# Kernel tuning notes

Hardware: AMD Instinct MI355X
Metric: run time of the kernel (lower is better)

The kernel has to match this reference:

```python
import jax, jax.numpy as jnp
import numpy as np
import math

B, D_MODEL, EMB, ORDER, SEQ = 4, 64, 33, 64, 256
TARGET, FAST_PCT, SLOW_PCT = 0.01, 0.3, 1.5


def _pos_emb(L, emb_dim):
    # PositionalEmbedding: t in [0,1], complex exponential bands
    t = jnp.linspace(0.0, 1.0, L)[None, :, None]                     # [1,L,1]
    bands = (emb_dim - 1) // 2
    t_r = jnp.linspace(0.0, L - 1.0, L)[None, :, None]
    w = 2.0 * math.pi * t_r / L
    f = jnp.linspace(1e-4, bands - 1.0, bands)[None, None]
    zc = jnp.exp(-1j * f * w)
    z = jnp.concatenate([t, zc.real, zc.imag], axis=-1)              # [1,L,emb_dim]
    return z.astype(jnp.float32), t.astype(jnp.float32)


def setup_inputs() -> dict:
    key = jax.random.key(0)
    ks = jax.random.split(key, 24)
    z, _ = _pos_emb(SEQ, EMB)

    def lin(k, fan_in, fan_out):
        return jax.random.normal(k, (fan_in, fan_out), jnp.float32) / np.sqrt(fan_in)

    inp = {
        'x': jax.random.normal(ks[0], (B, D_MODEL, SEQ, SEQ), jnp.float32),
        'z': z,
        'Xw1': lin(ks[1], EMB, ORDER), 'Xb1': jax.random.normal(ks[2], (ORDER,), jnp.float32) * 0.02,
        'Xw2': lin(ks[3], ORDER, ORDER), 'Xb2': jax.random.normal(ks[4], (ORDER,), jnp.float32) * 0.02,
        'Xw3': lin(ks[5], ORDER, ORDER), 'Xb3': jax.random.normal(ks[6], (ORDER,), jnp.float32) * 0.02,
        'Xwo': lin(ks[7], ORDER, D_MODEL),
        'Xfreq': jnp.ones((1, ORDER), jnp.float32),  # Sin freq, w=1, shared across layers
        'Yw1': lin(ks[8], EMB, ORDER), 'Yb1': jax.random.normal(ks[9], (ORDER,), jnp.float32) * 0.02,
        'Yw2': lin(ks[10], ORDER, ORDER), 'Yb2': jax.random.normal(ks[11], (ORDER,), jnp.float32) * 0.02,
        'Yw3': lin(ks[12], ORDER, ORDER), 'Yb3': jax.random.normal(ks[13], (ORDER,), jnp.float32) * 0.02,
        'Ywo': lin(ks[14], ORDER, D_MODEL),
        'Yfreq': jnp.ones((1, ORDER), jnp.float32),
        'bias': jax.random.normal(ks[15], (D_MODEL,), jnp.float32),
        'L': SEQ,
    }
    return inp


def _implicit_filter(z, w1, b1, w2, b2, w3, b3, wo, freq, t, deltas):
    # MLP with shared Sin activation, then exponential modulation (shift=0)
    h = jnp.sin(freq * (z @ w1 + b1))
    h = jnp.sin(freq * (h @ w2 + b2))
    h = jnp.sin(freq * (h @ w3 + b3))
    h = h @ wo                                   # [1,L,d_model]
    decay = jnp.exp(-t * jnp.abs(deltas))        # [1,L,d_model]
    return h * decay


def reference(x, z, Xw1, Xb1, Xw2, Xb2, Xw3, Xb3, Xwo, Xfreq,
              Yw1, Yb1, Yw2, Yb2, Yw3, Yb3, Ywo, Yfreq, bias, L):
    d_model = x.shape[1]
    t = jnp.linspace(0.0, 1.0, L)[None, :, None].astype(jnp.float32)
    max_dec = math.log(TARGET) / FAST_PCT
    min_dec = math.log(TARGET) / SLOW_PCT
    deltas = jnp.linspace(min_dec, max_dec, d_model)[None, None].astype(jnp.float32)

    hx = _implicit_filter(z, Xw1, Xb1, Xw2, Xb2, Xw3, Xb3, Xwo, Xfreq, t, deltas)
    hy = _implicit_filter(z, Yw1, Yb1, Yw2, Yb2, Yw3, Yb3, Ywo, Yfreq, t, deltas)
    # separable outer-product 2D kernel: [1,L,L,d_model] -> [d_model,L,L]
    k = jnp.einsum('ijk,imk->ijmk', hx, hy)[0]
    k = jnp.transpose(k, (2, 0, 1))

    fft_size = 2 * L
    k_f = jnp.fft.rfft2(k, s=(fft_size, fft_size)) / fft_size       # [D, 2L, L+1]
    u_f = jnp.fft.rfft2(x.astype(jnp.float32), s=(fft_size, fft_size))  # [B, D, 2L, L+1]
    y = jnp.fft.irfft2(u_f * k_f, s=(fft_size, fft_size))[..., :L, :L]
    out = y + x * bias[:, None, None]
    return out.astype(x.dtype)
```

## Files before the change

kernel.cpp:

```cpp
#include <hip/hip_runtime.h>

#define SL 256
#define RSTRIDE 312

typedef _Float16 f16;
typedef _Float16 f16x8 __attribute__((ext_vector_type(8)));
typedef _Float16 f16x4 __attribute__((ext_vector_type(4)));
typedef float f32x4 __attribute__((ext_vector_type(4)));

__global__ __launch_bounds__(64) void k_filters(
    const float* __restrict__ z,
    const float* __restrict__ Xw1, const float* __restrict__ Xb1,
    const float* __restrict__ Xw2, const float* __restrict__ Xb2,
    const float* __restrict__ Xw3, const float* __restrict__ Xb3,
    const float* __restrict__ Xwo, const float* __restrict__ Xfreq,
    const float* __restrict__ Yw1, const float* __restrict__ Yb1,
    const float* __restrict__ Yw2, const float* __restrict__ Yb2,
    const float* __restrict__ Yw3, const float* __restrict__ Yb3,
    const float* __restrict__ Ywo, const float* __restrict__ Yfreq,
    f16* __restrict__ hxT, f16* __restrict__ hyT)
{
    const int l = blockIdx.x;
    const int sel = blockIdx.y;
    const int t = threadIdx.x;
    const float* w1 = sel ? Yw1 : Xw1;  const float* b1 = sel ? Yb1 : Xb1;
    const float* w2 = sel ? Yw2 : Xw2;  const float* b2 = sel ? Yb2 : Xb2;
    const float* w3 = sel ? Yw3 : Xw3;  const float* b3 = sel ? Yb3 : Xb3;
    const float* wo = sel ? Ywo : Xwo;  const float* freq = sel ? Yfreq : Xfreq;
    f16* hT = sel ? hyT : hxT;

    __shared__ float zb[33];
    __shared__ float ha[64];
    __shared__ float hb[64];

    if (t < 33) zb[t] = z[l * 33 + t];
    __syncthreads();

    const float fr = freq[t];
    float s = b1[t];
    for (int k = 0; k < 33; ++k) s += zb[k] * w1[k * 64 + t];
    ha[t] = sinf(fr * s);
    __syncthreads();

    s = b2[t];
    for (int k = 0; k < 64; ++k) s += ha[k] * w2[k * 64 + t];
    hb[t] = sinf(fr * s);
    __syncthreads();

    s = b3[t];
    for (int k = 0; k < 64; ++k) s += hb[k] * w3[k * 64 + t];
    ha[t] = sinf(fr * s);
    __syncthreads();

    s = 0.f;
    for (int k = 0; k < 64; ++k) s += ha[k] * wo[k * 64 + t];

    const float MIN_DEC = -3.0701134573253937f;
    const float MAX_DEC = -15.350567286626968f;
    float ad = fabsf(MIN_DEC + (MAX_DEC - MIN_DEC) * ((float)t / 63.0f));
    float tl = (float)l / 255.0f;
    hT[t * 256 + l] = (f16)(s * expf(-tl * ad));
}

__device__ __forceinline__ f16x8 cvt8(float4 a, float4 b)
{
    f16x8 h;
    h[0] = (f16)a.x; h[1] = (f16)a.y; h[2] = (f16)a.z; h[3] = (f16)a.w;
    h[4] = (f16)b.x; h[5] = (f16)b.y; h[6] = (f16)b.z; h[7] = (f16)b.w;
    return h;
}

template<int NT>
__device__ __forceinline__ void build_R(f16* R, const f16* __restrict__ hc,
                                        int tid)
{
    for (int idx = tid; idx < 8 * RSTRIDE; idx += NT) {
        int c = idx / RSTRIDE;
        int k = idx - c * RSTRIDE;
        int u = k + c;
        R[idx] = (u <= 255) ? hc[255 - u] : (f16)0.f;
    }
}

__global__ __launch_bounds__(1024, 4) void k_one(
    const float* __restrict__ x, const f16* __restrict__ hxT,
    const f16* __restrict__ hyT, const float* __restrict__ bias,
    float* __restrict__ out)
{
    extern __shared__ __align__(16) f16 smem[];
    f16* tmp = smem;
    f16* Ry  = smem + 256 * 256;
    f16* Rx  = Ry + 8 * RSTRIDE;

    const int bd = blockIdx.x;
    const int d  = bd & 63;
    const int tid  = threadIdx.x;
    const int lane = tid & 63;
    const int wave = tid >> 6;
    const int ln   = lane & 15;
    const int quad = lane >> 4;

    const float* xbd = x + (size_t)bd * (SL * SL);

    build_R<1024>(Ry, hyT + d * 256, tid);

    f32x4 acc[16];
#pragma unroll
    for (int a = 0; a < 16; ++a) acc[a] = (f32x4){0.f, 0.f, 0.f, 0.f};

    __syncthreads();

    {
        const float* xr = xbd + (wave * 16 + ln) * SL + quad * 8;
        float4 a0 = *(const float4*)xr;
        float4 a1 = *(const float4*)(xr + 4);

#pragma unroll
        for (int s = 0; s < 8; ++s) {
            const int q0 = s * 32;
            f16x8 af = cvt8(a0, a1);
            if (s + 1 < 8) {
                a0 = *(const float4*)(xr + q0 + 32);
                a1 = *(const float4*)(xr + q0 + 36);
            }
#pragma unroll
            for (int c8 = 0; c8 < 16; ++c8) {
                if (32 * s <= c8 * 16 + 15) {
                    int j = c8 * 16 + ln;
                    int s0 = 255 - j + q0 + quad * 8;
                    int c = s0 & 7;
                    f16x8 bf = *(const f16x8*)&Ry[c * RSTRIDE + (s0 - c)];
                    acc[c8] = __builtin_amdgcn_mfma_f32_16x16x32_f16(
                        af, bf, acc[c8], 0, 0, 0);
                }
            }
        }

#pragma unroll
        for (int c8 = 0; c8 < 16; ++c8) {
            int jl = c8 * 16 + ln;
            int pb = wave * 16 + quad * 4;
            f32x4 a = acc[c8];
            f16x4 v;
            v[0] = (f16)a[0]; v[1] = (f16)a[1];
            v[2] = (f16)a[2]; v[3] = (f16)a[3];
            *(f16x4*)&tmp[jl * 256 + (pb ^ ((jl & 7) << 3))] = v;
        }
    }

    build_R<1024>(Rx, hxT + d * 256, tid);
#pragma unroll
    for (int a = 0; a < 16; ++a) acc[a] = (f32x4){0.f, 0.f, 0.f, 0.f};

    __syncthreads();

    const int igrp = wave & 3;
    const int jgrp = wave >> 2;
    const int nst = (igrp + 1) * 2;
    for (int s = 0; s < nst; ++s) {
        const int p0 = s * 32;
        f16x8 af[4];
#pragma unroll
        for (int rt = 0; rt < 4; ++rt) {
            int jl = jgrp * 64 + rt * 16 + ln;
            int off = (p0 + quad * 8) ^ ((jl & 7) << 3);
            af[rt] = *(const f16x8*)&tmp[jl * 256 + off];
        }
#pragma unroll
        for (int ct = 0; ct < 4; ++ct) {
            if (p0 <= igrp * 64 + ct * 16 + 15) {
                int i = igrp * 64 + ct * 16 + ln;
                int s0 = 255 - i + p0 + quad * 8;
                int c = s0 & 7;
                f16x8 bf = *(const f16x8*)&Rx[c * RSTRIDE + (s0 - c)];
#pragma unroll
                for (int rt = 0; rt < 4; ++rt)
                    acc[rt * 4 + ct] = __builtin_amdgcn_mfma_f32_16x16x32_f16(
                        af[rt], bf, acc[rt * 4 + ct], 0, 0, 0);
            }
        }
    }

    const float bv = bias[d];
    const float sc = 1.0f / 512.0f;
    float* obd = out + (size_t)bd * (SL * SL);
#pragma unroll
    for (int rt = 0; rt < 4; ++rt)
#pragma unroll
        for (int ct = 0; ct < 4; ++ct) {
            int i = igrp * 64 + ct * 16 + ln;
            int j = jgrp * 64 + rt * 16 + quad * 4;
            f32x4 a = acc[rt * 4 + ct];
            float4 xv = *(const float4*)(xbd + i * SL + j);
            float4 o;
            o.x = a[0] * sc + xv.x * bv;
            o.y = a[1] * sc + xv.y * bv;
            o.z = a[2] * sc + xv.z * bv;
            o.w = a[3] * sc + xv.w * bv;
            *(float4*)(obd + i * SL + j) = o;
        }
}

template<int J0>
__device__ __forceinline__ void phase1(
    const float* __restrict__ xr0, const float* __restrict__ xr1,
    const f16* __restrict__ R, f32x4 (&acc)[16], int ln, int quad)
{
    constexpr int QS = (J0 == 0) ? 4 : 8;
    float4 a0 = *(const float4*)xr0;
    float4 a1 = *(const float4*)(xr0 + 4);
    float4 b0 = *(const float4*)xr1;
    float4 b1 = *(const float4*)(xr1 + 4);

#pragma unroll
    for (int s = 0; s < QS; ++s) {
        const int q0 = s * 32;
        f16x8 af0 = cvt8(a0, a1);
        f16x8 af1 = cvt8(b0, b1);
        if (s + 1 < QS) {
            a0 = *(const float4*)(xr0 + q0 + 32);
            a1 = *(const float4*)(xr0 + q0 + 36);
            b0 = *(const float4*)(xr1 + q0 + 32);
            b1 = *(const float4*)(xr1 + q0 + 36);
        }
#pragma unroll
        for (int c8 = 0; c8 < 8; ++c8) {
            if (32 * s <= J0 + c8 * 16 + 15) {
                int j = J0 + c8 * 16 + ln;
                int s0 = 255 - j + q0 + quad * 8;
                int c = s0 & 7;
                f16x8 bf = *(const f16x8*)&R[c * RSTRIDE + (s0 - c)];
                acc[c8] = __builtin_amdgcn_mfma_f32_16x16x32_f16(
                    af0, bf, acc[c8], 0, 0, 0);
                acc[8 + c8] = __builtin_amdgcn_mfma_f32_16x16x32_f16(
                    af1, bf, acc[8 + c8], 0, 0, 0);
            }
        }
    }
}

__global__ __launch_bounds__(512, 4) void k_fused(
    const float* __restrict__ x, const f16* __restrict__ hxT,
    const f16* __restrict__ hyT, const float* __restrict__ bias,
    float* __restrict__ out)
{
    const int bd = blockIdx.x & 255;
    const int j0 = (blockIdx.x >> 8) << 7;
    const int d  = bd & 63;
    const int tid  = threadIdx.x;
    const int lane = tid & 63;
    const int wave = tid >> 6;
    const int ln   = lane & 15;
    const int quad = lane >> 4;

    __shared__ __align__(16) f16 tmp[128 * 256];
    __shared__ __align__(16) f16 R[8 * RSTRIDE];

    const float* xbd = x + (size_t)bd * (SL * SL);

    build_R<512>(R, hyT + d * 256, tid);

    f32x4 acc[16];
#pragma unroll
    for (int a = 0; a < 16; ++a) acc[a] = (f32x4){0.f, 0.f, 0.f, 0.f};

    __syncthreads();

    {
        const float* xr0 = xbd + (wave * 32 + ln) * SL + quad * 8;
        const float* xr1 = xr0 + 16 * SL;
        if (j0 == 0) phase1<0>(xr0, xr1, R, acc, ln, quad);
        else         phase1<128>(xr0, xr1, R, acc, ln, quad);

#pragma unroll
        for (int r = 0; r < 2; ++r)
#pragma unroll
            for (int c8 = 0; c8 < 8; ++c8) {
                int jl = c8 * 16 + ln;
                int pb = wave * 32 + r * 16 + quad * 4;
                f32x4 a = acc[r * 8 + c8];
                f16x4 v;
                v[0] = (f16)a[0]; v[1] = (f16)a[1];
                v[2] = (f16)a[2]; v[3] = (f16)a[3];
                *(f16x4*)&tmp[jl * 256 + (pb ^ ((jl & 7) << 3))] = v;
            }
    }

    __syncthreads();
    build_R<512>(R, hxT + d * 256, tid);
#pragma unroll
    for (int a = 0; a < 16; ++a) acc[a] = (f32x4){0.f, 0.f, 0.f, 0.f};
    __syncthreads();

    const int igrp = wave & 3;
    const int jgrp = wave >> 2;
    const int nst = (igrp + 1) * 2;
    for (int s = 0; s < nst; ++s) {
        const int p0 = s * 32;
        f16x8 af[4];
#pragma unroll
        for (int rt = 0; rt < 4; ++rt) {
            int jl = jgrp * 64 + rt * 16 + ln;
            int off = (p0 + quad * 8) ^ ((jl & 7) << 3);
            af[rt] = *(const f16x8*)&tmp[jl * 256 + off];
        }
#pragma unroll
        for (int ct = 0; ct < 4; ++ct) {
            if (p0 <= igrp * 64 + ct * 16 + 15) {
                int i = igrp * 64 + ct * 16 + ln;
                int s0 = 255 - i + p0 + quad * 8;
                int c = s0 & 7;
                f16x8 bf = *(const f16x8*)&R[c * RSTRIDE + (s0 - c)];
#pragma unroll
                for (int rt = 0; rt < 4; ++rt)
                    acc[rt * 4 + ct] = __builtin_amdgcn_mfma_f32_16x16x32_f16(
                        af[rt], bf, acc[rt * 4 + ct], 0, 0, 0);
            }
        }
    }

    const float bv = bias[d];
    const float sc = 1.0f / 512.0f;
    float* obd = out + (size_t)bd * (SL * SL);
#pragma unroll
    for (int rt = 0; rt < 4; ++rt)
#pragma unroll
        for (int ct = 0; ct < 4; ++ct) {
            int i = igrp * 64 + ct * 16 + ln;
            int j = j0 + jgrp * 64 + rt * 16 + quad * 4;
            f32x4 a = acc[rt * 4 + ct];
            float4 xv = *(const float4*)(xbd + i * SL + j);
            float4 o;
            o.x = a[0] * sc + xv.x * bv;
            o.y = a[1] * sc + xv.y * bv;
            o.z = a[2] * sc + xv.z * bv;
            o.w = a[3] * sc + xv.w * bv;
            *(float4*)(obd + i * SL + j) = o;
        }
}

extern "C" void kernel_launch(void* const* d_in, const int* in_sizes, int n_in,
                              void* d_out, int out_size, void* d_ws, size_t ws_size,
                              hipStream_t stream)
{
    (void)in_sizes; (void)n_in; (void)out_size; (void)ws_size;
    const float* x     = (const float*)d_in[0];
    const float* z     = (const float*)d_in[1];
    const float* Xw1   = (const float*)d_in[2];
    const float* Xb1   = (const float*)d_in[3];
    const float* Xw2   = (const float*)d_in[4];
    const float* Xb2   = (const float*)d_in[5];
    const float* Xw3   = (const float*)d_in[6];
    const float* Xb3   = (const float*)d_in[7];
    const float* Xwo   = (const float*)d_in[8];
    const float* Xfreq = (const float*)d_in[9];
    const float* Yw1   = (const float*)d_in[10];
    const float* Yb1   = (const float*)d_in[11];
    const float* Yw2   = (const float*)d_in[12];
    const float* Yb2   = (const float*)d_in[13];
    const float* Yw3   = (const float*)d_in[14];
    const float* Yb3   = (const float*)d_in[15];
    const float* Ywo   = (const float*)d_in[16];
    const float* Yfreq = (const float*)d_in[17];
    const float* bias  = (const float*)d_in[18];

    f16* hxT = (f16*)d_ws;
    f16* hyT = hxT + 64 * 256;

    k_filters<<<dim3(256, 2), 64, 0, stream>>>(
        z, Xw1, Xb1, Xw2, Xb2, Xw3, Xb3, Xwo, Xfreq,
        Yw1, Yb1, Yw2, Yb2, Yw3, Yb3, Ywo, Yfreq, hxT, hyT);

    const int dyn_lds = (256 * 256 + 2 * 8 * RSTRIDE) * (int)sizeof(f16);
    static hipError_t attr_rc = hipFuncSetAttribute(
        (const void*)k_one, hipFuncAttributeMaxDynamicSharedMemorySize, dyn_lds);

    if (attr_rc == hipSuccess) {
        k_one<<<256, 1024, dyn_lds, stream>>>(x, hxT, hyT, bias, (float*)d_out);
    } else {
        k_fused<<<512, 512, 0, stream>>>(x, hxT, hyT, bias, (float*)d_out);
    }
}
```

Measured before the change: 166.8 us.

## Split k_one into two column-chunk phases with double-buffered intermediate

Replaces the single-pass kernel, which ran the full row convolution into a 256x256 LDS buffer and then the full column convolution, with a kernel that processes the output in two 128-column chunks. Each chunk gets its own LDS buffer. Both Toeplitz tables are built up front and the x loads for the next chunk are issued before the current phase-2 work, aiming to overlap global loads with MFMA work. Waves are regrouped into 8 row groups by 2 column groups, which balances the triangular work differently. The cost is more barriers, some x rows loaded twice, and higher register pressure from prefetched data.

```diff
diff --git a/kernel.cpp b/kernel.cpp
--- a/kernel.cpp
+++ b/kernel.cpp
@@ -82,15 +82,104 @@
     }
 }
 
-__global__ __launch_bounds__(1024, 4) void k_one(
+template<int JC>
+__device__ __forceinline__ void p1_work(
+    const f16x8* axs, const f16* __restrict__ Ry, f16* __restrict__ buf,
+    int wave, int ln, int quad)
+{
+    f32x4 acc[8];
+#pragma unroll
+    for (int t = 0; t < 8; ++t) acc[t] = (f32x4){0.f, 0.f, 0.f, 0.f};
+
+#pragma unroll
+    for (int s = 0; s <= 4 * JC + 3; ++s) {
+        const int q0 = s * 32;
+#pragma unroll
+        for (int c8 = 0; c8 < 8; ++c8) {
+            if (s <= 4 * JC + (c8 >> 1)) {
+                const int j = JC * 128 + c8 * 16 + ln;
+                const int s0 = 255 - j + q0 + quad * 8;
+                const int c = s0 & 7;
+                f16x8 bf = *(const f16x8*)&Ry[c * RSTRIDE + (s0 - c)];
+                acc[c8] = __builtin_amdgcn_mfma_f32_16x16x32_f16(
+                    axs[s], bf, acc[c8], 0, 0, 0);
+            }
+        }
+    }
+#pragma unroll
+    for (int c8 = 0; c8 < 8; ++c8) {
+        const int jl = c8 * 16 + ln;
+        const int pb = wave * 16 + quad * 4;
+        f32x4 a = acc[c8];
+        f16x4 v;
+        v[0] = (f16)a[0]; v[1] = (f16)a[1];
+        v[2] = (f16)a[2]; v[3] = (f16)a[3];
+        *(f16x4*)&buf[jl * 256 + (pb ^ ((jl & 7) << 3))] = v;
+    }
+}
+
+template<int JC>
+__device__ __forceinline__ void p2_chunk(
+    const f16* __restrict__ buf, const f16* __restrict__ Rx,
+    const float* __restrict__ xbd, float* __restrict__ obd, float bv,
+    int igrp, int jgrp, int ln, int quad)
+{
+    f32x4 acc[8];
+#pragma unroll
+    for (int t = 0; t < 8; ++t) acc[t] = (f32x4){0.f, 0.f, 0.f, 0.f};
+
+    const int nst = igrp + 1;
+    for (int s = 0; s < nst; ++s) {
+        const int p0 = s * 32;
+        f16x8 af[4];
+#pragma unroll
+        for (int jt = 0; jt < 4; ++jt) {
+            const int jl = jgrp * 64 + jt * 16 + ln;
+            const int off = (p0 + quad * 8) ^ ((jl & 7) << 3);
+            af[jt] = *(const f16x8*)&buf[jl * 256 + off];
+        }
+#pragma unroll
+        for (int ct = 0; ct < 2; ++ct) {
+            const int i = igrp * 32 + ct * 16 + ln;
+            const int s0 = 255 - i + p0 + quad * 8;
+            const int c = s0 & 7;
+            f16x8 bf = *(const f16x8*)&Rx[c * RSTRIDE + (s0 - c)];
+#pragma unroll
+            for (int jt = 0; jt < 4; ++jt)
+                acc[ct * 4 + jt] = __builtin_amdgcn_mfma_f32_16x16x32_f16(
+                    af[jt], bf, acc[ct * 4 + jt], 0, 0, 0);
+        }
+    }
+
+    const float sc = 1.0f / 512.0f;
+#pragma unroll
+    for (int ct = 0; ct < 2; ++ct) {
+        const int i = igrp * 32 + ct * 16 + ln;
+#pragma unroll
+        for (int jt = 0; jt < 4; ++jt) {
+            const int j = JC * 128 + jgrp * 64 + jt * 16 + quad * 4;
+            f32x4 a = acc[ct * 4 + jt];
+            float4 xv = *(const float4*)(xbd + i * SL + j);
+            float4 o;
+            o.x = a[0] * sc + xv.x * bv;
+            o.y = a[1] * sc + xv.y * bv;
+            o.z = a[2] * sc + xv.z * bv;
+            o.w = a[3] * sc + xv.w * bv;
+            *(float4*)(obd + i * SL + j) = o;
+        }
+    }
+}
+
+__global__ __launch_bounds__(1024, 4) void k_pipe(
     const float* __restrict__ x, const f16* __restrict__ hxT,
     const f16* __restrict__ hyT, const float* __restrict__ bias,
     float* __restrict__ out)
 {
     extern __shared__ __align__(16) f16 smem[];
-    f16* tmp = smem;
-    f16* Ry  = smem + 256 * 256;
-    f16* Rx  = Ry + 8 * RSTRIDE;
+    f16* buf0 = smem;
+    f16* buf1 = smem + 128 * 256;
+    f16* Ry   = smem + 2 * 128 * 256;
+    f16* Rx   = Ry + 8 * RSTRIDE;
 
     const int bd = blockIdx.x;
     const int d  = bd & 63;
@@ -99,106 +188,57 @@
     const int wave = tid >> 6;
     const int ln   = lane & 15;
     const int quad = lane >> 4;
+    const int igrp = wave >> 1;
+    const int jgrp = wave & 1;
 
     const float* xbd = x + (size_t)bd * (SL * SL);
+    float* obd = out + (size_t)bd * (SL * SL);
 
     build_R<1024>(Ry, hyT + d * 256, tid);
-
-    f32x4 acc[16];
-#pragma unroll
-    for (int a = 0; a < 16; ++a) acc[a] = (f32x4){0.f, 0.f, 0.f, 0.f};
-
-    __syncthreads();
-
+    build_R<1024>(Rx, hxT + d * 256, tid);
+
+    const float* xr = xbd + (wave * 16 + ln) * SL + quad * 8;
+    const float bv = bias[d];
+
+    float4 p[8];
+#pragma unroll
+    for (int s = 0; s < 4; ++s) {
+        p[2 * s]     = *(const float4*)(xr + s * 32);
+        p[2 * s + 1] = *(const float4*)(xr + s * 32 + 4);
+    }
     {
-        const float* xr = xbd + (wave * 16 + ln) * SL + quad * 8;
-        float4 a0 = *(const float4*)xr;
-        float4 a1 = *(const float4*)(xr + 4);
-
-#pragma unroll
-        for (int s = 0; s < 8; ++s) {
-            const int q0 = s * 32;
-            f16x8 af = cvt8(a0, a1);
-            if (s + 1 < 8) {
-                a0 = *(const float4*)(xr + q0 + 32);
-                a1 = *(const float4*)(xr + q0 + 36);
-            }
-#pragma unroll
-            for (int c8 = 0; c8 < 16; ++c8) {
-                if (32 * s <= c8 * 16 + 15) {
-                    int j = c8 * 16 + ln;
-                    int s0 = 255 - j + q0 + quad * 8;
-                    int c = s0 & 7;
-                    f16x8 bf = *(const f16x8*)&Ry[c * RSTRIDE + (s0 - c)];
-                    acc[c8] = __builtin_amdgcn_mfma_f32_16x16x32_f16(
-                        af, bf, acc[c8], 0, 0, 0);
-                }
-            }
-        }
-
-#pragma unroll
-        for (int c8 = 0; c8 < 16; ++c8) {
-            int jl = c8 * 16 + ln;
-            int pb = wave * 16 + quad * 4;
-            f32x4 a = acc[c8];
-            f16x4 v;
-            v[0] = (f16)a[0]; v[1] = (f16)a[1];
-            v[2] = (f16)a[2]; v[3] = (f16)a[3];
-            *(f16x4*)&tmp[jl * 256 + (pb ^ ((jl & 7) << 3))] = v;
-        }
-    }
-
-    build_R<1024>(Rx, hxT + d * 256, tid);
-#pragma unroll
-    for (int a = 0; a < 16; ++a) acc[a] = (f32x4){0.f, 0.f, 0.f, 0.f};
-
-    __syncthreads();
-
-    const int igrp = wave & 3;
-    const int jgrp = wave >> 2;
-    const int nst = (igrp + 1) * 2;
-    for (int s = 0; s < nst; ++s) {
-        const int p0 = s * 32;
-        f16x8 af[4];
-#pragma unroll
-        for (int rt = 0; rt < 4; ++rt) {
-            int jl = jgrp * 64 + rt * 16 + ln;
-            int off = (p0 + quad * 8) ^ ((jl & 7) << 3);
-            af[rt] = *(const f16x8*)&tmp[jl * 256 + off];
-        }
-#pragma unroll
-        for (int ct = 0; ct < 4; ++ct) {
-            if (p0 <= igrp * 64 + ct * 16 + 15) {
-                int i = igrp * 64 + ct * 16 + ln;
-                int s0 = 255 - i + p0 + quad * 8;
-                int c = s0 & 7;
-                f16x8 bf = *(const f16x8*)&Rx[c * RSTRIDE + (s0 - c)];
-#pragma unroll
-                for (int rt = 0; rt < 4; ++rt)
-                    acc[rt * 4 + ct] = __builtin_amdgcn_mfma_f32_16x16x32_f16(
-                        af[rt], bf, acc[rt * 4 + ct], 0, 0, 0);
-            }
-        }
-    }
-
-    const float bv = bias[d];
-    const float sc = 1.0f / 512.0f;
-    float* obd = out + (size_t)bd * (SL * SL);
-#pragma unroll
-    for (int rt = 0; rt < 4; ++rt)
-#pragma unroll
-        for (int ct = 0; ct < 4; ++ct) {
-            int i = igrp * 64 + ct * 16 + ln;
-            int j = jgrp * 64 + rt * 16 + quad * 4;
-            f32x4 a = acc[rt * 4 + ct];
-            float4 xv = *(const float4*)(xbd + i * SL + j);
-            float4 o;
-            o.x = a[0] * sc + xv.x * bv;
-            o.y = a[1] * sc + xv.y * bv;
-            o.z = a[2] * sc + xv.z * bv;
-            o.w = a[3] * sc + xv.w * bv;
-            *(float4*)(obd + i * SL + j) = o;
-        }
+        f16x8 axs[4];
+#pragma unroll
+        for (int s = 0; s < 4; ++s) axs[s] = cvt8(p[2 * s], p[2 * s + 1]);
+        __syncthreads();
+        p1_work<0>(axs, Ry, buf0, wave, ln, quad);
+    }
+    __syncthreads();
+
+#pragma unroll
+    for (int s = 0; s < 4; ++s) {
+        p[2 * s]     = *(const float4*)(xr + 128 + s * 32);
+        p[2 * s + 1] = *(const float4*)(xr + 128 + s * 32 + 4);
+    }
+
+    p2_chunk<0>(buf0, Rx, xbd, obd, bv, igrp, jgrp, ln, quad);
+
+    {
+        f16x8 axs[8];
+#pragma unroll
+        for (int s = 0; s < 4; ++s) axs[4 + s] = cvt8(p[2 * s], p[2 * s + 1]);
+#pragma unroll
+        for (int s = 0; s < 4; ++s) {
+            p[2 * s]     = *(const float4*)(xr + s * 32);
+            p[2 * s + 1] = *(const float4*)(xr + s * 32 + 4);
+        }
+#pragma unroll
+        for (int s = 0; s < 4; ++s) axs[s] = cvt8(p[2 * s], p[2 * s + 1]);
+        p1_work<1>(axs, Ry, buf1, wave, ln, quad);
+    }
+    __syncthreads();
+
+    p2_chunk<1>(buf1, Rx, xbd, obd, bv, igrp, jgrp, ln, quad);
 }
 
 template<int J0>
@@ -371,12 +411,12 @@
         z, Xw1, Xb1, Xw2, Xb2, Xw3, Xb3, Xwo, Xfreq,
         Yw1, Yb1, Yw2, Yb2, Yw3, Yb3, Ywo, Yfreq, hxT, hyT);
 
-    const int dyn_lds = (256 * 256 + 2 * 8 * RSTRIDE) * (int)sizeof(f16);
+    const int dyn_lds = (2 * 128 * 256 + 2 * 8 * RSTRIDE) * (int)sizeof(f16);
     static hipError_t attr_rc = hipFuncSetAttribute(
-        (const void*)k_one, hipFuncAttributeMaxDynamicSharedMemorySize, dyn_lds);
+        (const void*)k_pipe, hipFuncAttributeMaxDynamicSharedMemorySize, dyn_lds);
 
     if (attr_rc == hipSuccess) {
-        k_one<<<256, 1024, dyn_lds, stream>>>(x, hxT, hyT, bias, (float*)d_out);
+        k_pipe<<<256, 1024, dyn_lds, stream>>>(x, hxT, hyT, bias, (float*)d_out);
     } else {
         k_fused<<<512, 512, 0, stream>>>(x, hxT, hyT, bias, (float*)d_out);
     }
```

Result: slower. 171.4 us (+2.8%).
